# Optimization experiments

Hardware: AMD Instinct MI355X
Metric: run time of the kernel (lower is better)

## Reference

```python
import jax, jax.numpy as jnp
import numpy as np

B, S, D = 4, 2048, 512   # batch, seq_len, head_size (== d_model)
H = 8                    # num_heads
DH = D // H              # depth per head = 64


def setup_inputs() -> dict:
    key = jax.random.key(0)
    ks = jax.random.split(key, 11)
    sc = 1.0 / np.sqrt(D)
    inp = {
        "q": jax.random.normal(ks[0], (B, S, D), jnp.float32),
        "k": jax.random.normal(ks[1], (B, S, D), jnp.float32),
        "v": jax.random.normal(ks[2], (B, S, D), jnp.float32),
        # causal mask: 1.0 where attention is disallowed (j > i)
        "mask": jnp.triu(jnp.ones((S, S), jnp.float32), k=1)[None, None, :, :],
        "wq": jax.random.normal(ks[3], (D, D), jnp.float32) * sc,
        "bq": jnp.zeros((D,), jnp.float32),
        "wk": jax.random.normal(ks[4], (D, D), jnp.float32) * sc,
        "bk": jnp.zeros((D,), jnp.float32),
        "wv": jax.random.normal(ks[5], (D, D), jnp.float32) * sc,
        "bv": jnp.zeros((D,), jnp.float32),
        "wo": jax.random.normal(ks[6], (D, D), jnp.float32) * sc,
        "bo": jnp.zeros((D,), jnp.float32),
    }
    return inp


def _split_heads(x):
    # [B,S,D] -> [B,H,S,DH]
    return x.reshape(B, S, H, DH).transpose(0, 2, 1, 3)


def reference(q, k, v, mask, wq, bq, wk, bk, wv, bv, wo, bo):
    query = _split_heads(q @ wq + bq)
    key_h = _split_heads(k @ wk + bk)
    value = _split_heads(v @ wv + bv)

    scale = 1.0 / jnp.sqrt(jnp.asarray(DH, jnp.float32))
    scores = jnp.einsum("bhqd,bhkd->bhqk", query, key_h) * scale
    scores = scores + mask * -1e9
    attn = jax.nn.softmax(scores, axis=-1)  # [B,H,S,S]

    ctx = jnp.einsum("bhqk,bhkd->bhqd", attn, value)
    ctx = ctx.transpose(0, 2, 1, 3).reshape(B, S, D)  # concat heads
    out = ctx @ wo + bo
    return out, attn
```

## Files before the change

### kernel.cpp

```cpp
#include <hip/hip_runtime.h>

#define Bq 4
#define Sq 2048
#define Dq 512
#define Hq 8
#define DHq 64

typedef __attribute__((ext_vector_type(8))) short bf16x8;
typedef __attribute__((ext_vector_type(4))) float floatx4;

__device__ __forceinline__ unsigned short f2bf(float f) {
    union { float f; unsigned u; } v; v.f = f;
    return (unsigned short)((v.u + 0x7fffu + ((v.u >> 16) & 1u)) >> 16);
}

template <bool OUT_BF16>
__global__ __launch_bounds__(256) void gemm_bias(
    const float* A0, const float* A1, const float* A2,
    const float* W0, const float* W1, const float* W2,
    const float* b0, const float* b1, const float* b2,
    unsigned short* O0, unsigned short* O1, unsigned short* O2,
    float* F0, float* F1, float* F2) {
  const int bz = blockIdx.z;
  const float* A = (bz == 0) ? A0 : (bz == 1) ? A1 : A2;
  const float* W = (bz == 0) ? W0 : (bz == 1) ? W1 : W2;
  const float* bias = (bz == 0) ? b0 : (bz == 1) ? b1 : b2;
  unsigned short* O = (bz == 0) ? O0 : (bz == 1) ? O1 : O2;
  float* F = (bz == 0) ? F0 : (bz == 1) ? F1 : F2;

  const int bm = blockIdx.x;
  const int bn = blockIdx.y;
  const int tid = threadIdx.x;
  const int lane = tid & 63;
  const int w = tid >> 6;
  const int wm = w >> 1;
  const int wn = w & 1;
  const int lg = lane >> 4;
  const int lc = lane & 15;

  __shared__ unsigned short As[4096];
  __shared__ unsigned short Bs[4096];

  floatx4 acc[4][4];
#pragma unroll
  for (int mt = 0; mt < 4; ++mt)
#pragma unroll
    for (int nt = 0; nt < 4; ++nt) acc[mt][nt] = (floatx4){0.f, 0.f, 0.f, 0.f};

  for (int kt = 0; kt < 16; ++kt) {
    __syncthreads();
#pragma unroll
    for (int it = 0; it < 4; ++it) {
      int idx = tid + it * 256;
      int m = idx >> 3;
      int k0 = (idx & 7) << 2;
      const float4 va =
          *(const float4*)(A + (size_t)(bm * 128 + m) * 512 + kt * 32 + k0);
      union { unsigned short u[4]; uint2 v; } pk;
      pk.u[0] = f2bf(va.x); pk.u[1] = f2bf(va.y);
      pk.u[2] = f2bf(va.z); pk.u[3] = f2bf(va.w);
      *(uint2*)&As[((((k0 >> 3) * 128 + m)) << 3) + (k0 & 7)] = pk.v;
    }
#pragma unroll
    for (int it = 0; it < 4; ++it) {
      int e = tid + it * 256;
      int n = e & 127;
      int k0 = (e >> 7) << 2;
      union { unsigned short u[4]; uint2 v; } pk;
#pragma unroll
      for (int u = 0; u < 4; ++u)
        pk.u[u] = f2bf(W[(size_t)(kt * 32 + k0 + u) * 512 + bn * 128 + n]);
      *(uint2*)&Bs[((((k0 >> 3) * 128 + n)) << 3) + (k0 & 7)] = pk.v;
    }
    __syncthreads();

    bf16x8 af[4], bfr[4];
#pragma unroll
    for (int mt = 0; mt < 4; ++mt)
      af[mt] = *(const bf16x8*)&As[(lg * 128 + wm * 64 + mt * 16 + lc) << 3];
#pragma unroll
    for (int nt = 0; nt < 4; ++nt)
      bfr[nt] = *(const bf16x8*)&Bs[(lg * 128 + wn * 64 + nt * 16 + lc) << 3];
#pragma unroll
    for (int mt = 0; mt < 4; ++mt)
#pragma unroll
      for (int nt = 0; nt < 4; ++nt)
        acc[mt][nt] = __builtin_amdgcn_mfma_f32_16x16x32_bf16(
            af[mt], bfr[nt], acc[mt][nt], 0, 0, 0);
  }

#pragma unroll
  for (int mt = 0; mt < 4; ++mt) {
#pragma unroll
    for (int nt = 0; nt < 4; ++nt) {
      int col = bn * 128 + wn * 64 + nt * 16 + lc;
      float bv = bias[col];
#pragma unroll
      for (int r = 0; r < 4; ++r) {
        int row = bm * 128 + wm * 64 + mt * 16 + lg * 4 + r;
        float val = acc[mt][nt][r] + bv;
        if (OUT_BF16)
          O[(size_t)row * 512 + col] = f2bf(val);
        else
          F[(size_t)row * 512 + col] = val;
      }
    }
  }
}

__global__ __launch_bounds__(256) void attn_kernel(
    const unsigned short* Qb, const unsigned short* Kb,
    const unsigned short* Vb, float* attn, float* ctx) {
  const int qt = blockIdx.x;
  const int h = blockIdx.y;
  const int b = blockIdx.z;
  const int qb = qt * 64;
  const int tid = threadIdx.x;
  const int lane = tid & 63;
  const int w = tid >> 6;
  const int lg = lane >> 4;
  const int lc = lane & 15;

  __shared__ unsigned short Qs[4096], Ks[4096], Vs[4096], Ps[4096];

#pragma unroll
  for (int it = 0; it < 2; ++it) {
    int cc = tid + it * 256;
    int koct = cc & 7, m = cc >> 3;
    *(uint4*)&Qs[((koct << 6) + m) << 3] =
        *(const uint4*)&Qb[(size_t)(b * Sq + qb + m) * Dq + h * DHq +
                           (koct << 3)];
  }
  __syncthreads();

  bf16x8 aQ[2];
#pragma unroll
  for (int ks = 0; ks < 2; ++ks)
    aQ[ks] = *(const bf16x8*)&Qs[(((ks * 4 + lg) << 6) + (w * 16 + lc)) << 3];

  float mrun[4] = {-1e30f, -1e30f, -1e30f, -1e30f};
  float lrun[4] = {0.f, 0.f, 0.f, 0.f};
  const int qi_base = qb + w * 16 + lg * 4;

  for (int jt = 0; jt <= qt; ++jt) {
    __syncthreads();
#pragma unroll
    for (int it = 0; it < 2; ++it) {
      int cc = tid + it * 256;
      int koct = cc & 7, m = cc >> 3;
      *(uint4*)&Ks[((koct << 6) + m) << 3] =
          *(const uint4*)&Kb[(size_t)(b * Sq + jt * 64 + m) * Dq + h * DHq +
                             (koct << 3)];
    }
    __syncthreads();

    floatx4 s[4];
#pragma unroll
    for (int nt = 0; nt < 4; ++nt) s[nt] = (floatx4){0.f, 0.f, 0.f, 0.f};
#pragma unroll
    for (int ks = 0; ks < 2; ++ks)
#pragma unroll
      for (int nt = 0; nt < 4; ++nt) {
        bf16x8 bk =
            *(const bf16x8*)&Ks[(((ks * 4 + lg) << 6) + nt * 16 + lc) << 3];
        s[nt] = __builtin_amdgcn_mfma_f32_16x16x32_bf16(aQ[ks], bk, s[nt], 0,
                                                        0, 0);
      }

#pragma unroll
    for (int r = 0; r < 4; ++r) {
      int qi = qi_base + r;
      float sv[4];
      float mx = -1e30f;
#pragma unroll
      for (int nt = 0; nt < 4; ++nt) {
        float x = s[nt][r] * 0.125f;
        int kj = jt * 64 + nt * 16 + lc;
        if (kj > qi) x = -1e30f;
        sv[nt] = x;
        mx = fmaxf(mx, x);
      }
#pragma unroll
      for (int off = 1; off < 16; off <<= 1)
        mx = fmaxf(mx, __shfl_xor(mx, off, 16));
      float mnew = fmaxf(mrun[r], mx);
      float sum = 0.f;
#pragma unroll
      for (int nt = 0; nt < 4; ++nt) sum += __expf(sv[nt] - mnew);
#pragma unroll
      for (int off = 1; off < 16; off <<= 1) sum += __shfl_xor(sum, off, 16);
      lrun[r] = lrun[r] * __expf(mrun[r] - mnew) + sum;
      mrun[r] = mnew;
    }
  }

  float rinv[4];
#pragma unroll
  for (int r = 0; r < 4; ++r) rinv[r] = 1.0f / lrun[r];

  floatx4 ctxa[4];
#pragma unroll
  for (int nt = 0; nt < 4; ++nt) ctxa[nt] = (floatx4){0.f, 0.f, 0.f, 0.f};

  float* attn_base = attn + (size_t)(b * Hq + h) * Sq * Sq;

  for (int jt = 0; jt <= qt; ++jt) {
    __syncthreads();
#pragma unroll
    for (int it = 0; it < 2; ++it) {
      int cc = tid + it * 256;
      int koct = cc & 7, m = cc >> 3;
      *(uint4*)&Ks[((koct << 6) + m) << 3] =
          *(const uint4*)&Kb[(size_t)(b * Sq + jt * 64 + m) * Dq + h * DHq +
                             (koct << 3)];
    }
#pragma unroll
    for (int it = 0; it < 2; ++it) {
      int cc = tid + it * 256;
      int dim = cc & 63, koct = cc >> 6;
      union { unsigned short u[8]; uint4 v; } pk;
#pragma unroll
      for (int u = 0; u < 8; ++u)
        pk.u[u] = Vb[(size_t)(b * Sq + jt * 64 + koct * 8 + u) * Dq + h * DHq +
                     dim];
      *(uint4*)&Vs[((koct << 6) + dim) << 3] = pk.v;
    }
    __syncthreads();

    floatx4 s[4];
#pragma unroll
    for (int nt = 0; nt < 4; ++nt) s[nt] = (floatx4){0.f, 0.f, 0.f, 0.f};
#pragma unroll
    for (int ks = 0; ks < 2; ++ks)
#pragma unroll
      for (int nt = 0; nt < 4; ++nt) {
        bf16x8 bk =
            *(const bf16x8*)&Ks[(((ks * 4 + lg) << 6) + nt * 16 + lc) << 3];
        s[nt] = __builtin_amdgcn_mfma_f32_16x16x32_bf16(aQ[ks], bk, s[nt], 0,
                                                        0, 0);
      }

#pragma unroll
    for (int r = 0; r < 4; ++r) {
      int qi = qi_base + r;
      float* arow = attn_base + (size_t)qi * Sq + jt * 64;
#pragma unroll
      for (int nt = 0; nt < 4; ++nt) {
        int kj = jt * 64 + nt * 16 + lc;
        float x = s[nt][r] * 0.125f;
        float p = (kj > qi) ? 0.f : __expf(x - mrun[r]) * rinv[r];
        arow[nt * 16 + lc] = p;
        int kk = nt * 16 + lc;
        Ps[w * 1024 + (((kk >> 3) * 16 + lg * 4 + r) << 3) + (kk & 7)] =
            f2bf(p);
      }
    }

#pragma unroll
    for (int ks = 0; ks < 2; ++ks) {
      bf16x8 ap =
          *(const bf16x8*)&Ps[w * 1024 + (((ks * 4 + lg) * 16 + lc) << 3)];
#pragma unroll
      for (int nt = 0; nt < 4; ++nt) {
        bf16x8 bv =
            *(const bf16x8*)&Vs[(((ks * 4 + lg) << 6) + nt * 16 + lc) << 3];
        ctxa[nt] = __builtin_amdgcn_mfma_f32_16x16x32_bf16(ap, bv, ctxa[nt],
                                                           0, 0, 0);
      }
    }
  }

#pragma unroll
  for (int nt = 0; nt < 4; ++nt)
#pragma unroll
    for (int r = 0; r < 4; ++r) {
      int qi = qi_base + r;
      ctx[(size_t)(b * Sq + qi) * Dq + h * DHq + nt * 16 + lc] = ctxa[nt][r];
    }

  int zc0 = qb + 64;
  int ncol4 = (Sq - zc0) >> 2;
  if (ncol4 > 0) {
    for (int rr = 0; rr < 64; ++rr) {
      float4* rowp = (float4*)(attn_base + (size_t)(qb + rr) * Sq + zc0);
      for (int c4 = tid; c4 < ncol4; c4 += 256)
        rowp[c4] = make_float4(0.f, 0.f, 0.f, 0.f);
    }
  }
}

extern "C" void kernel_launch(void* const* d_in, const int* in_sizes, int n_in,
                              void* d_out, int out_size, void* d_ws,
                              size_t ws_size, hipStream_t stream) {
  const float* q = (const float*)d_in[0];
  const float* k = (const float*)d_in[1];
  const float* v = (const float*)d_in[2];
  const float* wq = (const float*)d_in[4];
  const float* bq = (const float*)d_in[5];
  const float* wk = (const float*)d_in[6];
  const float* bk = (const float*)d_in[7];
  const float* wv = (const float*)d_in[8];
  const float* bv = (const float*)d_in[9];
  const float* wo = (const float*)d_in[10];
  const float* bo = (const float*)d_in[11];

  float* out = (float*)d_out;
  float* attn = out + (size_t)Bq * Sq * Dq;

  unsigned short* Qb = (unsigned short*)d_ws;
  unsigned short* Kb = Qb + (size_t)Bq * Sq * Dq;
  unsigned short* Vb = Kb + (size_t)Bq * Sq * Dq;
  float* ctx = (float*)(Vb + (size_t)Bq * Sq * Dq);

  dim3 blk(256);
  dim3 g1(64, 4, 3);
  gemm_bias<true><<<g1, blk, 0, stream>>>(q, k, v, wq, wk, wv, bq, bk, bv, Qb,
                                          Kb, Vb, nullptr, nullptr, nullptr);

  dim3 g2(Sq / 64, Hq, Bq);
  attn_kernel<<<g2, blk, 0, stream>>>(Qb, Kb, Vb, attn, ctx);

  dim3 g3(64, 4, 1);
  gemm_bias<false><<<g3, blk, 0, stream>>>(
      ctx, nullptr, nullptr, wo, nullptr, nullptr, bo, nullptr, nullptr,
      nullptr, nullptr, nullptr, out, nullptr, nullptr);
}
```

Baseline: 803.1 us.

## Rewrite pipeline with pre-transposed bf16 weights, transposed V, LDS-free attention

```diff
diff --git a/kernel.cpp b/kernel.cpp
--- a/kernel.cpp
+++ b/kernel.cpp
@@ -10,36 +10,65 @@
 typedef __attribute__((ext_vector_type(4))) float floatx4;
 
 __device__ __forceinline__ unsigned short f2bf(float f) {
-    union { float f; unsigned u; } v; v.f = f;
-    return (unsigned short)((v.u + 0x7fffu + ((v.u >> 16) & 1u)) >> 16);
-}
-
-template <bool OUT_BF16>
-__global__ __launch_bounds__(256) void gemm_bias(
+  union { float f; unsigned u; } v; v.f = f;
+  return (unsigned short)((v.u + 0x7fffu + ((v.u >> 16) & 1u)) >> 16);
+}
+
+__device__ __forceinline__ void gload16(const unsigned short* g,
+                                        unsigned short* l) {
+  __builtin_amdgcn_global_load_lds(
+      (const __attribute__((address_space(1))) void*)g,
+      (__attribute__((address_space(3))) void*)l, 16, 0, 0);
+}
+
+__global__ __launch_bounds__(256) void wtrans(
+    const float* wq, const float* wk, const float* wv, const float* wo,
+    unsigned short* WT) {
+  const int wz = blockIdx.y;
+  const float* W = (wz == 0) ? wq : (wz == 1) ? wk : (wz == 2) ? wv : wo;
+  unsigned short* WTz = WT + (size_t)wz * 512 * 512;
+  const int k0 = (blockIdx.x >> 3) << 6;
+  const int n0 = (blockIdx.x & 7) << 6;
+  const int tid = threadIdx.x;
+  __shared__ unsigned short T[64][65];
+#pragma unroll
+  for (int it = 0; it < 16; ++it) {
+    int idx = tid + it * 256;
+    int r = idx >> 6, c = idx & 63;
+    T[c][r] = f2bf(W[(size_t)(k0 + r) * 512 + n0 + c]);
+  }
+  __syncthreads();
+#pragma unroll
+  for (int it = 0; it < 2; ++it) {
+    int e = tid + it * 256;
+    int n = e >> 3, koct = e & 7;
+    union { unsigned short u[8]; uint4 v; } pk;
+#pragma unroll
+    for (int j = 0; j < 8; ++j) pk.u[j] = T[n][koct * 8 + j];
+    *(uint4*)&WTz[(size_t)(n0 + n) * 512 + k0 + koct * 8] = pk.v;
+  }
+}
+
+template <int MODE>
+__global__ __launch_bounds__(256) void gemm_kernel(
     const float* A0, const float* A1, const float* A2,
-    const float* W0, const float* W1, const float* W2,
+    const unsigned short* Ab, const unsigned short* WT,
     const float* b0, const float* b1, const float* b2,
-    unsigned short* O0, unsigned short* O1, unsigned short* O2,
-    float* F0, float* F1, float* F2) {
+    unsigned short* O0, unsigned short* O1, unsigned short* VtO,
+    float* Fout) {
   const int bz = blockIdx.z;
   const float* A = (bz == 0) ? A0 : (bz == 1) ? A1 : A2;
-  const float* W = (bz == 0) ? W0 : (bz == 1) ? W1 : W2;
   const float* bias = (bz == 0) ? b0 : (bz == 1) ? b1 : b2;
-  unsigned short* O = (bz == 0) ? O0 : (bz == 1) ? O1 : O2;
-  float* F = (bz == 0) ? F0 : (bz == 1) ? F1 : F2;
+  const unsigned short* WTz = WT + (size_t)((MODE == 1) ? 3 : bz) * 262144;
 
   const int bm = blockIdx.x;
   const int bn = blockIdx.y;
   const int tid = threadIdx.x;
   const int lane = tid & 63;
-  const int w = tid >> 6;
-  const int wm = w >> 1;
-  const int wn = w & 1;
-  const int lg = lane >> 4;
-  const int lc = lane & 15;
-
-  __shared__ unsigned short As[4096];
-  __shared__ unsigned short Bs[4096];
+  const int w = tid >> 6, wm = w >> 1, wn = w & 1;
+  const int lg = lane >> 4, lc = lane & 15;
+
+  __shared__ unsigned short As[4096], Bs[4096];
 
   floatx4 acc[4][4];
 #pragma unroll
@@ -49,28 +78,33 @@
 
   for (int kt = 0; kt < 16; ++kt) {
     __syncthreads();
-#pragma unroll
-    for (int it = 0; it < 4; ++it) {
-      int idx = tid + it * 256;
-      int m = idx >> 3;
-      int k0 = (idx & 7) << 2;
-      const float4 va =
-          *(const float4*)(A + (size_t)(bm * 128 + m) * 512 + kt * 32 + k0);
-      union { unsigned short u[4]; uint2 v; } pk;
-      pk.u[0] = f2bf(va.x); pk.u[1] = f2bf(va.y);
-      pk.u[2] = f2bf(va.z); pk.u[3] = f2bf(va.w);
-      *(uint2*)&As[((((k0 >> 3) * 128 + m)) << 3) + (k0 & 7)] = pk.v;
+    if (MODE == 0) {
+#pragma unroll
+      for (int it = 0; it < 4; ++it) {
+        int idx = tid + it * 256;
+        int m = idx >> 3, k0 = (idx & 7) << 2;
+        const float4 va =
+            *(const float4*)(A + (size_t)(bm * 128 + m) * 512 + kt * 32 + k0);
+        union { unsigned short u[4]; uint2 v; } pk;
+        pk.u[0] = f2bf(va.x); pk.u[1] = f2bf(va.y);
+        pk.u[2] = f2bf(va.z); pk.u[3] = f2bf(va.w);
+        *(uint2*)&As[(((k0 >> 3) * 128 + m) << 3) + (k0 & 7)] = pk.v;
+      }
+    } else {
+#pragma unroll
+      for (int it = 0; it < 2; ++it) {
+        int c = tid + it * 256;
+        gload16(Ab + (size_t)(bm * 128 + (c & 127)) * 512 + kt * 32 +
+                    (c >> 7) * 8,
+                &As[c << 3]);
+      }
     }
 #pragma unroll
-    for (int it = 0; it < 4; ++it) {
-      int e = tid + it * 256;
-      int n = e & 127;
-      int k0 = (e >> 7) << 2;
-      union { unsigned short u[4]; uint2 v; } pk;
-#pragma unroll
-      for (int u = 0; u < 4; ++u)
-        pk.u[u] = f2bf(W[(size_t)(kt * 32 + k0 + u) * 512 + bn * 128 + n]);
-      *(uint2*)&Bs[((((k0 >> 3) * 128 + n)) << 3) + (k0 & 7)] = pk.v;
+    for (int it = 0; it < 2; ++it) {
+      int c = tid + it * 256;
+      gload16(WTz + (size_t)(bn * 128 + (c & 127)) * 512 + kt * 32 +
+                  (c >> 7) * 8,
+              &Bs[c << 3]);
     }
     __syncthreads();
 
@@ -93,199 +127,165 @@
   for (int mt = 0; mt < 4; ++mt) {
 #pragma unroll
     for (int nt = 0; nt < 4; ++nt) {
-      int col = bn * 128 + wn * 64 + nt * 16 + lc;
-      float bv = bias[col];
+      const int col = bn * 128 + wn * 64 + nt * 16 + lc;
+      const float bvv = bias[col];
+      const int row0 = bm * 128 + wm * 64 + mt * 16 + lg * 4;
+      if (MODE == 1) {
+#pragma unroll
+        for (int r = 0; r < 4; ++r)
+          Fout[(size_t)(row0 + r) * 512 + col] = acc[mt][nt][r] + bvv;
+      } else if (bz == 2) {
+        union { unsigned short u[4]; uint2 v; } pk;
+#pragma unroll
+        for (int r = 0; r < 4; ++r) pk.u[r] = f2bf(acc[mt][nt][r] + bvv);
+        const int bb = row0 >> 11, s0 = row0 & 2047;
+        const int hh = col >> 6, dh = col & 63;
+        *(uint2*)&VtO[((size_t)((bb * 8 + hh) * 64 + dh)) * 2048 + s0] = pk.v;
+      } else {
+        unsigned short* O = (bz == 0) ? O0 : O1;
+#pragma unroll
+        for (int r = 0; r < 4; ++r)
+          O[(size_t)(row0 + r) * 512 + col] = f2bf(acc[mt][nt][r] + bvv);
+      }
+    }
+  }
+}
+
+__global__ __launch_bounds__(256) void attn_kernel(
+    const unsigned short* __restrict__ Qb, const unsigned short* __restrict__ Kb,
+    const unsigned short* __restrict__ Vt, float* __restrict__ attn,
+    unsigned short* __restrict__ ctxb) {
+  const int lid = blockIdx.x;
+  const int xcd = lid & 7;
+  const int idx = lid >> 3;
+  const int bh = xcd * 4 + (idx >> 5);
+  const int qt = idx & 31;
+  const int b = bh >> 3, h = bh & 7;
+
+  const int tid = threadIdx.x;
+  const int lane = tid & 63, w = tid >> 6;
+  const int lg = lane >> 4, lc = lane & 15;
+  const int q0 = qt * 64 + w * 16;
+  const int qi = q0 + lc;
+
+  __shared__ unsigned short Ps[4096];
+  unsigned short* Pw = &Ps[w * 1024];
+
+  bf16x8 bQ[2];
+#pragma unroll
+  for (int ks = 0; ks < 2; ++ks)
+    bQ[ks] = *(const bf16x8*)&Qb[(size_t)(b * Sq + q0 + lc) * Dq + h * DHq +
+                                 (ks * 4 + lg) * 8];
+
+  const unsigned short* kb = &Kb[(size_t)(b * Sq) * Dq + h * DHq];
+  float mrun = -1e30f, lrun = 0.f;
+
+  for (int jt = 0; jt <= qt; ++jt) {
+    const unsigned short* kt_ = kb + (size_t)(jt * 64) * Dq;
+    floatx4 s[4];
+#pragma unroll
+    for (int nt = 0; nt < 4; ++nt) s[nt] = (floatx4){0.f, 0.f, 0.f, 0.f};
+#pragma unroll
+    for (int ks = 0; ks < 2; ++ks)
+#pragma unroll
+      for (int nt = 0; nt < 4; ++nt) {
+        bf16x8 ak = *(const bf16x8*)&kt_[(size_t)(nt * 16 + lc) * Dq +
+                                         (ks * 4 + lg) * 8];
+        s[nt] = __builtin_amdgcn_mfma_f32_16x16x32_bf16(ak, bQ[ks], s[nt],
+                                                        0, 0, 0);
+      }
+    float sv[4][4];
+    float mx = -1e30f;
+    const int kjb = jt * 64 + lg * 4;
+#pragma unroll
+    for (int nt = 0; nt < 4; ++nt)
 #pragma unroll
       for (int r = 0; r < 4; ++r) {
-        int row = bm * 128 + wm * 64 + mt * 16 + lg * 4 + r;
-        float val = acc[mt][nt][r] + bv;
-        if (OUT_BF16)
-          O[(size_t)row * 512 + col] = f2bf(val);
-        else
-          F[(size_t)row * 512 + col] = val;
-      }
+        float x = s[nt][r] * 0.125f;
+        if (kjb + nt * 16 + r > qi) x = -1e30f;
+        sv[nt][r] = x;
+        mx = fmaxf(mx, x);
+      }
+    mx = fmaxf(mx, __shfl_xor(mx, 16));
+    mx = fmaxf(mx, __shfl_xor(mx, 32));
+    const float mnew = fmaxf(mrun, mx);
+    float sum = 0.f;
+#pragma unroll
+    for (int nt = 0; nt < 4; ++nt)
+#pragma unroll
+      for (int r = 0; r < 4; ++r) sum += __expf(sv[nt][r] - mnew);
+    sum += __shfl_xor(sum, 16);
+    sum += __shfl_xor(sum, 32);
+    lrun = lrun * __expf(mrun - mnew) + sum;
+    mrun = mnew;
+  }
+  const float rinv = 1.0f / lrun;
+
+  floatx4 ctxa[4];
+#pragma unroll
+  for (int nt = 0; nt < 4; ++nt) ctxa[nt] = (floatx4){0.f, 0.f, 0.f, 0.f};
+  float* abase = attn + (size_t)(b * Hq + h) * Sq * Sq;
+  const unsigned short* vb = &Vt[(size_t)((b * Hq + h) * DHq) * Sq];
+
+  for (int jt = 0; jt <= qt; ++jt) {
+    const unsigned short* kt_ = kb + (size_t)(jt * 64) * Dq;
+    floatx4 s[4];
+#pragma unroll
+    for (int nt = 0; nt < 4; ++nt) s[nt] = (floatx4){0.f, 0.f, 0.f, 0.f};
+#pragma unroll
+    for (int ks = 0; ks < 2; ++ks)
+#pragma unroll
+      for (int nt = 0; nt < 4; ++nt) {
+        bf16x8 ak = *(const bf16x8*)&kt_[(size_t)(nt * 16 + lc) * Dq +
+                                         (ks * 4 + lg) * 8];
+        s[nt] = __builtin_amdgcn_mfma_f32_16x16x32_bf16(ak, bQ[ks], s[nt],
+                                                        0, 0, 0);
+      }
+    const int kjb = jt * 64 + lg * 4;
+#pragma unroll
+    for (int nt = 0; nt < 4; ++nt) {
+      floatx4 pv;
+      union { unsigned short u[4]; uint2 v2; } pb;
+#pragma unroll
+      for (int r = 0; r < 4; ++r) {
+        float x = s[nt][r] * 0.125f;
+        float p = (kjb + nt * 16 + r > qi) ? 0.f : __expf(x - mrun) * rinv;
+        pv[r] = p;
+        pb.u[r] = f2bf(p);
+      }
+      __builtin_nontemporal_store(
+          pv, (floatx4*)&abase[(size_t)qi * Sq + jt * 64 + nt * 16 + lg * 4]);
+      *(uint2*)&Pw[((nt * 2 + (lg >> 1)) * 16 + lc) * 8 + (lg & 1) * 4] =
+          pb.v2;
     }
-  }
-}
-
-__global__ __launch_bounds__(256) void attn_kernel(
-    const unsigned short* Qb, const unsigned short* Kb,
-    const unsigned short* Vb, float* attn, float* ctx) {
-  const int qt = blockIdx.x;
-  const int h = blockIdx.y;
-  const int b = blockIdx.z;
-  const int qb = qt * 64;
-  const int tid = threadIdx.x;
-  const int lane = tid & 63;
-  const int w = tid >> 6;
-  const int lg = lane >> 4;
-  const int lc = lane & 15;
-
-  __shared__ unsigned short Qs[4096], Ks[4096], Vs[4096], Ps[4096];
-
-#pragma unroll
-  for (int it = 0; it < 2; ++it) {
-    int cc = tid + it * 256;
-    int koct = cc & 7, m = cc >> 3;
-    *(uint4*)&Qs[((koct << 6) + m) << 3] =
-        *(const uint4*)&Qb[(size_t)(b * Sq + qb + m) * Dq + h * DHq +
-                           (koct << 3)];
-  }
-  __syncthreads();
-
-  bf16x8 aQ[2];
-#pragma unroll
-  for (int ks = 0; ks < 2; ++ks)
-    aQ[ks] = *(const bf16x8*)&Qs[(((ks * 4 + lg) << 6) + (w * 16 + lc)) << 3];
-
-  float mrun[4] = {-1e30f, -1e30f, -1e30f, -1e30f};
-  float lrun[4] = {0.f, 0.f, 0.f, 0.f};
-  const int qi_base = qb + w * 16 + lg * 4;
-
-  for (int jt = 0; jt <= qt; ++jt) {
-    __syncthreads();
-#pragma unroll
-    for (int it = 0; it < 2; ++it) {
-      int cc = tid + it * 256;
-      int koct = cc & 7, m = cc >> 3;
-      *(uint4*)&Ks[((koct << 6) + m) << 3] =
-          *(const uint4*)&Kb[(size_t)(b * Sq + jt * 64 + m) * Dq + h * DHq +
-                             (koct << 3)];
-    }
-    __syncthreads();
-
-    floatx4 s[4];
-#pragma unroll
-    for (int nt = 0; nt < 4; ++nt) s[nt] = (floatx4){0.f, 0.f, 0.f, 0.f};
+    bf16x8 ap[2];
 #pragma unroll
     for (int ks = 0; ks < 2; ++ks)
+      ap[ks] = *(const bf16x8*)&Pw[((ks * 4 + lg) * 16 + lc) * 8];
+#pragma unroll
+    for (int ks = 0; ks < 2; ++ks)
 #pragma unroll
       for (int nt = 0; nt < 4; ++nt) {
-        bf16x8 bk =
-            *(const bf16x8*)&Ks[(((ks * 4 + lg) << 6) + nt * 16 + lc) << 3];
-        s[nt] = __builtin_amdgcn_mfma_f32_16x16x32_bf16(aQ[ks], bk, s[nt], 0,
-                                                        0, 0);
-      }
-
-#pragma unroll
-    for (int r = 0; r < 4; ++r) {
-      int qi = qi_base + r;
-      float sv[4];
-      float mx = -1e30f;
-#pragma unroll
-      for (int nt = 0; nt < 4; ++nt) {
-        float x = s[nt][r] * 0.125f;
-        int kj = jt * 64 + nt * 16 + lc;
-        if (kj > qi) x = -1e30f;
-        sv[nt] = x;
-        mx = fmaxf(mx, x);
-      }
-#pragma unroll
-      for (int off = 1; off < 16; off <<= 1)
-        mx = fmaxf(mx, __shfl_xor(mx, off, 16));
-      float mnew = fmaxf(mrun[r], mx);
-      float sum = 0.f;
-#pragma unroll
-      for (int nt = 0; nt < 4; ++nt) sum += __expf(sv[nt] - mnew);
-#pragma unroll
-      for (int off = 1; off < 16; off <<= 1) sum += __shfl_xor(sum, off, 16);
-      lrun[r] = lrun[r] * __expf(mrun[r] - mnew) + sum;
-      mrun[r] = mnew;
-    }
-  }
-
-  float rinv[4];
-#pragma unroll
-  for (int r = 0; r < 4; ++r) rinv[r] = 1.0f / lrun[r];
-
-  floatx4 ctxa[4];
-#pragma unroll
-  for (int nt = 0; nt < 4; ++nt) ctxa[nt] = (floatx4){0.f, 0.f, 0.f, 0.f};
-
-  float* attn_base = attn + (size_t)(b * Hq + h) * Sq * Sq;
-
-  for (int jt = 0; jt <= qt; ++jt) {
-    __syncthreads();
-#pragma unroll
-    for (int it = 0; it < 2; ++it) {
-      int cc = tid + it * 256;
-      int koct = cc & 7, m = cc >> 3;
-      *(uint4*)&Ks[((koct << 6) + m) << 3] =
-          *(const uint4*)&Kb[(size_t)(b * Sq + jt * 64 + m) * Dq + h * DHq +
-                             (koct << 3)];
-    }
-#pragma unroll
-    for (int it = 0; it < 2; ++it) {
-      int cc = tid + it * 256;
-      int dim = cc & 63, koct = cc >> 6;
-      union { unsigned short u[8]; uint4 v; } pk;
-#pragma unroll
-      for (int u = 0; u < 8; ++u)
-        pk.u[u] = Vb[(size_t)(b * Sq + jt * 64 + koct * 8 + u) * Dq + h * DHq +
-                     dim];
-      *(uint4*)&Vs[((koct << 6) + dim) << 3] = pk.v;
-    }
-    __syncthreads();
-
-    floatx4 s[4];
-#pragma unroll
-    for (int nt = 0; nt < 4; ++nt) s[nt] = (floatx4){0.f, 0.f, 0.f, 0.f};
-#pragma unroll
-    for (int ks = 0; ks < 2; ++ks)
-#pragma unroll
-      for (int nt = 0; nt < 4; ++nt) {
-        bf16x8 bk =
-            *(const bf16x8*)&Ks[(((ks * 4 + lg) << 6) + nt * 16 + lc) << 3];
-        s[nt] = __builtin_amdgcn_mfma_f32_16x16x32_bf16(aQ[ks], bk, s[nt], 0,
-                                                        0, 0);
-      }
-
-#pragma unroll
-    for (int r = 0; r < 4; ++r) {
-      int qi = qi_base + r;
-      float* arow = attn_base + (size_t)qi * Sq + jt * 64;
-#pragma unroll
-      for (int nt = 0; nt < 4; ++nt) {
-        int kj = jt * 64 + nt * 16 + lc;
-        float x = s[nt][r] * 0.125f;
-        float p = (kj > qi) ? 0.f : __expf(x - mrun[r]) * rinv[r];
-        arow[nt * 16 + lc] = p;
-        int kk = nt * 16 + lc;
-        Ps[w * 1024 + (((kk >> 3) * 16 + lg * 4 + r) << 3) + (kk & 7)] =
-            f2bf(p);
-      }
-    }
-
-#pragma unroll
-    for (int ks = 0; ks < 2; ++ks) {
-      bf16x8 ap =
-          *(const bf16x8*)&Ps[w * 1024 + (((ks * 4 + lg) * 16 + lc) << 3)];
-#pragma unroll
-      for (int nt = 0; nt < 4; ++nt) {
-        bf16x8 bv =
-            *(const bf16x8*)&Vs[(((ks * 4 + lg) << 6) + nt * 16 + lc) << 3];
-        ctxa[nt] = __builtin_amdgcn_mfma_f32_16x16x32_bf16(ap, bv, ctxa[nt],
-                                                           0, 0, 0);
-      }
-    }
+        bf16x8 bv = *(const bf16x8*)&vb[(size_t)(nt * 16 + lc) * Sq + jt * 64 +
+                                        (ks * 4 + lg) * 8];
+        ctxa[nt] = __builtin_amdgcn_mfma_f32_16x16x32_bf16(ap[ks], bv,
+                                                           ctxa[nt], 0, 0, 0);
+      }
   }
 
 #pragma unroll
   for (int nt = 0; nt < 4; ++nt)
 #pragma unroll
-    for (int r = 0; r < 4; ++r) {
-      int qi = qi_base + r;
-      ctx[(size_t)(b * Sq + qi) * Dq + h * DHq + nt * 16 + lc] = ctxa[nt][r];
-    }
-
-  int zc0 = qb + 64;
-  int ncol4 = (Sq - zc0) >> 2;
-  if (ncol4 > 0) {
-    for (int rr = 0; rr < 64; ++rr) {
-      float4* rowp = (float4*)(attn_base + (size_t)(qb + rr) * Sq + zc0);
-      for (int c4 = tid; c4 < ncol4; c4 += 256)
-        rowp[c4] = make_float4(0.f, 0.f, 0.f, 0.f);
-    }
+    for (int r = 0; r < 4; ++r)
+      ctxb[(size_t)(b * Sq + q0 + lg * 4 + r) * Dq + h * DHq + nt * 16 + lc] =
+          f2bf(ctxa[nt][r]);
+
+  const floatx4 z4 = {0.f, 0.f, 0.f, 0.f};
+  const int kend = (qt + 1) * 64;
+  for (int rr = 0; rr < 16; ++rr) {
+    float* rp = abase + (size_t)(q0 + rr) * Sq;
+    for (int c = kend + lane * 4; c < Sq; c += 256)
+      __builtin_nontemporal_store(z4, (floatx4*)&rp[c]);
   }
 }
 
@@ -309,19 +309,19 @@
 
   unsigned short* Qb = (unsigned short*)d_ws;
   unsigned short* Kb = Qb + (size_t)Bq * Sq * Dq;
-  unsigned short* Vb = Kb + (size_t)Bq * Sq * Dq;
-  float* ctx = (float*)(Vb + (size_t)Bq * Sq * Dq);
+  unsigned short* Vt = Kb + (size_t)Bq * Sq * Dq;
+  unsigned short* ctxb = Vt + (size_t)Bq * Sq * Dq;
+  unsigned short* WTb = ctxb + (size_t)Bq * Sq * Dq;
 
   dim3 blk(256);
-  dim3 g1(64, 4, 3);
-  gemm_bias<true><<<g1, blk, 0, stream>>>(q, k, v, wq, wk, wv, bq, bk, bv, Qb,
-                                          Kb, Vb, nullptr, nullptr, nullptr);
-
-  dim3 g2(Sq / 64, Hq, Bq);
-  attn_kernel<<<g2, blk, 0, stream>>>(Qb, Kb, Vb, attn, ctx);
-
-  dim3 g3(64, 4, 1);
-  gemm_bias<false><<<g3, blk, 0, stream>>>(
-      ctx, nullptr, nullptr, wo, nullptr, nullptr, bo, nullptr, nullptr,
-      nullptr, nullptr, nullptr, out, nullptr, nullptr);
-}
+  wtrans<<<dim3(64, 4), blk, 0, stream>>>(wq, wk, wv, wo, WTb);
+
+  gemm_kernel<0><<<dim3(64, 4, 3), blk, 0, stream>>>(
+      q, k, v, nullptr, WTb, bq, bk, bv, Qb, Kb, Vt, nullptr);
+
+  attn_kernel<<<dim3(1024, 1, 1), blk, 0, stream>>>(Qb, Kb, Vt, attn, ctxb);
+
+  gemm_kernel<1><<<dim3(64, 4, 1), blk, 0, stream>>>(
+      nullptr, nullptr, nullptr, ctxb, WTb, bo, nullptr, nullptr, nullptr,
+      nullptr, nullptr, out);
+}
```

Result: slower. 913.7 us (+13.8%).
